# Performance work log

Measured on AMD Instinct MI355X. Metric: run time of the kernel, lower is better.

## Reference

```python
import jax, jax.numpy as jnp
import numpy as np

D_MODEL = 1024
NHEAD = 16
HEAD_DIM = D_MODEL // NHEAD  # 64
THETA = 10000.0


def apply_rope(t):
    # t: [B, H, S, D]. Interleaved-pair RoPE (lucidrains rotary-embedding-torch
    # rotate_queries_or_keys), positions = arange(S), theta = 10000.
    B, H, S, D = t.shape
    inv_freq = 1.0 / (THETA ** (jnp.arange(0, D, 2, dtype=jnp.float32) / D))  # [D/2]
    ang = jnp.arange(S, dtype=jnp.float32)[:, None] * inv_freq               # [S, D/2]
    cos = jnp.cos(ang).astype(t.dtype)
    sin = jnp.sin(ang).astype(t.dtype)
    tp = t.reshape(B, H, S, D // 2, 2)
    x1, x2 = tp[..., 0], tp[..., 1]
    rot = jnp.stack([x1 * cos - x2 * sin, x1 * sin + x2 * cos], axis=-1)
    return rot.reshape(B, H, S, D)


def setup_inputs() -> dict:
    key = jax.random.key(0)
    k0, k1, k2, k3, k4 = jax.random.split(key, 5)
    B, Sx, Sc = 2, 2048, 2048
    sc = 0.02  # weight init scale
    return {
        "x": jax.random.normal(k0, (B, Sx, D_MODEL), jnp.float32),
        "context": jax.random.normal(k1, (B, Sc, D_MODEL), jnp.float32),
        "Wq": jax.random.normal(k2, (D_MODEL, D_MODEL), jnp.float32) * sc,
        "Wv": jax.random.normal(k3, (D_MODEL, D_MODEL), jnp.float32) * sc,
        "Wo": jax.random.normal(k4, (D_MODEL, D_MODEL), jnp.float32) * sc,
        "bo": jnp.zeros((D_MODEL,), jnp.float32),
        "x_pos": jnp.arange(B * Sx, dtype=jnp.int64).reshape(B, Sx) % Sx,
        "context_pos": jnp.arange(B * Sc, dtype=jnp.int64).reshape(B, Sc) % Sc,
    }


def reference(x, context, Wq, Wv, Wo, bo, x_pos, context_pos):
    # x_pos/context_pos are unused when both streams use the internal
    # RotaryEmbedding (is_imu1=is_imu2=True), matching the original forward.
    B, Sx, _ = x.shape
    Sc = context.shape[1]
    q = (x @ Wq.T).reshape(B, Sx, NHEAD, HEAD_DIM).transpose(0, 2, 1, 3)
    # NOTE: original code uses projq (not projk) for keys — replicated here.
    k = (context @ Wq.T).reshape(B, Sc, NHEAD, HEAD_DIM).transpose(0, 2, 1, 3)
    v = (context @ Wv.T).reshape(B, Sc, NHEAD, HEAD_DIM).transpose(0, 2, 1, 3)
    q = apply_rope(q)
    k = apply_rope(k)
    scale = 1.0 / jnp.sqrt(jnp.asarray(HEAD_DIM, q.dtype))
    attn = jax.nn.softmax(jnp.einsum("bhqd,bhkd->bhqk", q, k) * scale, axis=-1)
    out = jnp.einsum("bhqk,bhkd->bhqd", attn, v)            # [B,H,Sx,hd]
    out = out.transpose(0, 2, 1, 3).reshape(B, Sx, D_MODEL)  # [B,Sx,d_model]
    return out @ Wo.T + bo
```

## Files before the change

### kernel.cpp

```cpp
#include <hip/hip_runtime.h>
#include <cmath>


typedef __bf16 bf16x8 __attribute__((ext_vector_type(8)));
typedef __bf16 bf16x4 __attribute__((ext_vector_type(4)));
typedef float f32x4 __attribute__((ext_vector_type(4)));
typedef float f32x16 __attribute__((ext_vector_type(16)));
typedef unsigned u32x4v __attribute__((ext_vector_type(4)));

#define MFMA(A, B, C) __builtin_amdgcn_mfma_f32_16x16x32_bf16(A, B, C, 0, 0, 0)
#define MFMA32(A, B, C) __builtin_amdgcn_mfma_f32_32x32x16_bf16(A, B, C, 0, 0, 0)
#define GLL16(g, l)                                                        \
  __builtin_amdgcn_global_load_lds(                                        \
      (const __attribute__((address_space(1))) unsigned int*)(g),          \
      (__attribute__((address_space(3))) unsigned int*)(l), 16, 0, 0)

__global__ __launch_bounds__(256) void cvt_all_kernel(
    const float* __restrict__ x, const float* __restrict__ ctx,
    const float* __restrict__ Wq, const float* __restrict__ Wv,
    const float* __restrict__ Wo, __bf16* __restrict__ xb, __bf16* __restrict__ cb,
    __bf16* __restrict__ Wqb, __bf16* __restrict__ Wvb, __bf16* __restrict__ Wob) {
  int base = blockIdx.x * 512 + threadIdx.x;
  const float* src;
  __bf16* dst;
  int off;
  if (base < 1048576) { src = x; dst = xb; off = 0; }
  else if (base < 2097152) { src = ctx; dst = cb; off = 1048576; }
  else if (base < 2359296) { src = Wq; dst = Wqb; off = 2097152; }
  else if (base < 2621440) { src = Wv; dst = Wvb; off = 2359296; }
  else { src = Wo; dst = Wob; off = 2621440; }
#pragma unroll
  for (int jj = 0; jj < 2; jj++) {
    int j = base - off + jj * 256;
    float4 f = ((const float4*)src)[j];
    bf16x4 o;
    o[0] = (__bf16)f.x; o[1] = (__bf16)f.y; o[2] = (__bf16)f.z; o[3] = (__bf16)f.w;
    ((bf16x4*)dst)[j] = o;
  }
}

__global__ __launch_bounds__(256) void gemm_proj(const __bf16* __restrict__ A0,
                                                 const __bf16* __restrict__ W0,
                                                 void* __restrict__ outQ,
                                                 void* __restrict__ outK,
                                                 void* __restrict__ outV) {
  const int tid = threadIdx.x;
  const int wave = tid >> 6, lane = tid & 63, quad = lane >> 4, l15 = lane & 15;
  const int mw = wave >> 1, nw = wave & 1;

  const int id = blockIdx.x;
  int m0, n0;
  const __bf16* A;
  const __bf16* W;
  bool vmode;
  if (id < 512) {
    const int xcd = id & 7, j = id >> 3;
    m0 = (xcd * 8 + (j & 7)) * 128;
    n0 = (j >> 3) * 128;
    A = A0;
    W = W0;
    vmode = false;
  } else {
    const int vid = id - 512;
    const int xcd = vid & 7, j = vid >> 3;
    m0 = (xcd * 4 + (j & 3)) * 128;
    n0 = (j >> 2) * 128;
    A = A0 + (size_t)4096 * 1024;
    W = W0 + (size_t)1024 * 1024;
    vmode = true;
  }

  __shared__ __attribute__((aligned(16))) __bf16 As[3][4096];
  __shared__ __attribute__((aligned(16))) __bf16 Ws[3][4096];

  int goff[2];
#pragma unroll
  for (int jj = 0; jj < 2; jj++) {
    const int s = jj * 256 + tid;
    const int row = s >> 2;
    const int kcg = (s & 3) ^ ((row >> 1) & 3);
    goff[jj] = row * 1024 + kcg * 8;
  }
  const __bf16* Ag = A + (size_t)m0 * 1024;
  const __bf16* Wg = W + (size_t)n0 * 1024;
  const int ldsoff0 = wave * 512;
  const int ldsoff1 = 2048 + wave * 512;

  const int sw = (l15 >> 1) & 3;
  int afoff[4], wfoff[4];
#pragma unroll
  for (int t = 0; t < 4; t++) {
    afoff[t] = (mw * 64 + t * 16 + l15) * 32 + (quad ^ sw) * 8;
    wfoff[t] = (nw * 64 + t * 16 + l15) * 32 + (quad ^ sw) * 8;
  }

  f32x4 acc[4][4] = {};

  auto stage = [&](int buf, int k0) {
    GLL16(Ag + goff[0] + k0, &As[buf][ldsoff0]);
    GLL16(Ag + goff[1] + k0, &As[buf][ldsoff1]);
    GLL16(Wg + goff[0] + k0, &Ws[buf][ldsoff0]);
    GLL16(Wg + goff[1] + k0, &Ws[buf][ldsoff1]);
  };
  auto compute = [&](int buf) {
    bf16x8 af[4], wf[4];
#pragma unroll
    for (int t = 0; t < 4; t++) af[t] = *(const bf16x8*)&As[buf][afoff[t]];
#pragma unroll
    for (int t = 0; t < 4; t++) wf[t] = *(const bf16x8*)&Ws[buf][wfoff[t]];
#pragma unroll
    for (int mt = 0; mt < 4; mt++)
#pragma unroll
      for (int nt = 0; nt < 4; nt++) acc[mt][nt] = MFMA(af[mt], wf[nt], acc[mt][nt]);
  };

  stage(0, 0);
  stage(1, 32);
  int buf = 0;
  for (int c = 0; c < 32; c++) {
    __syncthreads();
    if (c + 2 < 32) {
      int nb = buf + 2;
      if (nb >= 3) nb -= 3;
      stage(nb, (c + 2) * 32);
    }
    compute(buf);
    buf = (buf == 2) ? 0 : buf + 1;
  }

  if (!vmode) {
    const int isK = (m0 >= 4096);
    __bf16* O = (__bf16*)(isK ? outK : outQ);
    const float qsc = isK ? 1.0f : 0.18033688f;
    const int mb = m0 & 4095;
#pragma unroll
    for (int nt = 0; nt < 4; nt++) {
      const int n = n0 + nw * 64 + nt * 16 + l15;
      const int h = n >> 6, d = n & 63, p = d >> 1;
      const float invf_rev =
          __builtin_amdgcn_exp2f(-((float)p * 0.41524101f + 2.6514961f));
#pragma unroll
      for (int mt = 0; mt < 4; mt++) {
#pragma unroll
        for (int r = 0; r < 4; r++) {
          const int row = mb + mw * 64 + mt * 16 + quad * 4 + r;
          const int s = row & 2047, b = row >> 11;
          float v = acc[mt][nt][r];
          float pv = __shfl_xor(v, 1, 64);
          float fr = __builtin_amdgcn_fractf((float)s * invf_rev);
          float sn = __builtin_amdgcn_sinf(fr);
          float cs = __builtin_amdgcn_cosf(fr);
          float res = (lane & 1) ? (pv * sn + v * cs) : (v * cs - pv * sn);
          O[((size_t)(b * 16 + h) * 2048 + s) * 64 + d] = (__bf16)(res * qsc);
        }
      }
    }
  } else {
    __bf16* O = (__bf16*)outV;
#pragma unroll
    for (int nt = 0; nt < 4; nt++) {
      const int n = n0 + nw * 64 + nt * 16 + l15;
      const int h = n >> 6, d = n & 63;
#pragma unroll
      for (int mt = 0; mt < 4; mt++) {
        const int rowb = m0 + mw * 64 + mt * 16 + quad * 4;
        const int s = rowb & 2047, b = rowb >> 11;
        bf16x4 o;
#pragma unroll
        for (int r = 0; r < 4; r++) o[r] = (__bf16)acc[mt][nt][r];
        *(bf16x4*)(O + ((size_t)(b * 16 + h) * 64 + d) * 2048 + s) = o;
      }
    }
  }
}

__global__ __launch_bounds__(256) void gemm_out(const __bf16* __restrict__ A,
                                                const __bf16* __restrict__ W,
                                                float* __restrict__ O,
                                                const float* __restrict__ bias) {
  const int tid = threadIdx.x;
  const int wave = tid >> 6, lane = tid & 63, quad = lane >> 4, l15 = lane & 15;
  const int mw = wave >> 1, nw = wave & 1;
  const int id = blockIdx.x;
  const int xcd = id & 7, j = id >> 3;
  const int m0 = (xcd * 4 + (j & 3)) * 128;
  const int n0 = (j >> 2) * 64;

  __shared__ __attribute__((aligned(16))) __bf16 As[3][4096];
  __shared__ __attribute__((aligned(16))) __bf16 Ws[3][2048];

  int goff[2];
#pragma unroll
  for (int jj = 0; jj < 2; jj++) {
    const int s = jj * 256 + tid;
    const int row = s >> 2;
    const int kcg = (s & 3) ^ ((row >> 1) & 3);
    goff[jj] = row * 1024 + kcg * 8;
  }
  const int wrow = tid >> 2;
  const int wkcg = (tid & 3) ^ ((wrow >> 1) & 3);
  const int goffw = wrow * 1024 + wkcg * 8;

  const __bf16* Ag = A + (size_t)m0 * 1024;
  const __bf16* Wg = W + (size_t)n0 * 1024;
  const int ldsoff0 = wave * 512;
  const int ldsoff1 = 2048 + wave * 512;

  const int sw = (l15 >> 1) & 3;
  int afoff[4], wfoff[2];
#pragma unroll
  for (int t = 0; t < 4; t++)
    afoff[t] = (mw * 64 + t * 16 + l15) * 32 + (quad ^ sw) * 8;
#pragma unroll
  for (int t = 0; t < 2; t++)
    wfoff[t] = (nw * 32 + t * 16 + l15) * 32 + (quad ^ sw) * 8;

  f32x4 acc[4][2] = {};

  auto stage = [&](int buf, int k0) {
    GLL16(Ag + goff[0] + k0, &As[buf][ldsoff0]);
    GLL16(Ag + goff[1] + k0, &As[buf][ldsoff1]);
    GLL16(Wg + goffw + k0, &Ws[buf][ldsoff0]);
  };
  auto compute = [&](int buf) {
    bf16x8 af[4], wf[2];
#pragma unroll
    for (int t = 0; t < 4; t++) af[t] = *(const bf16x8*)&As[buf][afoff[t]];
#pragma unroll
    for (int t = 0; t < 2; t++) wf[t] = *(const bf16x8*)&Ws[buf][wfoff[t]];
#pragma unroll
    for (int mt = 0; mt < 4; mt++)
#pragma unroll
      for (int nt = 0; nt < 2; nt++) acc[mt][nt] = MFMA(af[mt], wf[nt], acc[mt][nt]);
  };

  stage(0, 0);
  stage(1, 32);
  int buf = 0;
  for (int c = 0; c < 32; c++) {
    __syncthreads();
    if (c + 2 < 32) {
      int nb = buf + 2;
      if (nb >= 3) nb -= 3;
      stage(nb, (c + 2) * 32);
    }
    compute(buf);
    buf = (buf == 2) ? 0 : buf + 1;
  }

#pragma unroll
  for (int nt = 0; nt < 2; nt++) {
    const int n = n0 + nw * 32 + nt * 16 + l15;
    const float bv = bias[n];
#pragma unroll
    for (int mt = 0; mt < 4; mt++) {
#pragma unroll
      for (int r = 0; r < 4; r++) {
        const int row = m0 + mw * 64 + mt * 16 + quad * 4 + r;
        O[(size_t)row * 1024 + n] = acc[mt][nt][r] + bv;
      }
    }
  }
}

__global__ __launch_bounds__(512, 4) void attn_kernel(const __bf16* __restrict__ Q,
                                                      const __bf16* __restrict__ K,
                                                      const __bf16* __restrict__ Vt,
                                                      __bf16* __restrict__ Aout) {
  const int tid = threadIdx.x;
  const int wave = tid >> 6, lane = tid & 63;
  const int l31 = lane & 31, hi = lane >> 5;
  const int qg = wave >> 1, kg = wave & 1;
  const int id = blockIdx.x;
  const int j = id >> 3;
  const int bh = ((id & 7) << 2) | (j & 3);
  const int q0 = (j >> 2) << 7;

  const __bf16* Qb = Q + (size_t)bh * (2048 * 64);
  const __bf16* Kb = K + (size_t)bh * (2048 * 64);
  const __bf16* Vb = Vt + (size_t)bh * (64 * 2048);

  __shared__ __attribute__((aligned(16))) __bf16 Kbuf[4][4096];
  __shared__ __attribute__((aligned(16))) __bf16 Vbuf[4][4096];

  bf16x8 qf[4];
  {
    const __bf16* qp = Qb + (size_t)(q0 + qg * 32 + l31) * 64 + hi * 8;
#pragma unroll
    for (int i = 0; i < 4; i++) qf[i] = *(const bf16x8*)(qp + i * 16);
  }

  const int s0 = wave * 64 + lane;
  const int r0 = s0 >> 3, c0 = (s0 & 7) ^ (r0 & 7);
  const __bf16* kgp = Kb + r0 * 64 + c0 * 8;
  const __bf16* vgp = Vb + r0 * 2048 + c0 * 8;
  const int klds = wave * 512;

  int koff[4];
  {
    const int rk = kg * 32 + l31;
#pragma unroll
    for (int i = 0; i < 4; i++) koff[i] = rk * 64 + (((2 * i + hi) ^ (rk & 7)) * 8);
  }
  int voff[2][2];
#pragma unroll
  for (int dt = 0; dt < 2; dt++) {
    const int rv = dt * 32 + l31;
#pragma unroll
    for (int ks = 0; ks < 2; ks++)
      voff[dt][ks] = rv * 64 + (((kg * 4 + ks * 2 + hi) ^ (rv & 7)) * 8);
  }

  f32x4 rs4 = {};
  f32x16 oacc[2] = {};

  auto stage = [&](int buf, int kt) {
    GLL16(kgp + kt * 64, &Kbuf[buf][klds]);
    GLL16(vgp + kt, &Vbuf[buf][klds]);
  };

  auto compute = [&](int buf) {
    f32x16 s = {};
#pragma unroll
    for (int i = 0; i < 4; i++) {
      bf16x8 kf = *(const bf16x8*)&Kbuf[buf][koff[i]];
      s = MFMA32(kf, qf[i], s);
    }
    float pe[16];
#pragma unroll
    for (int r = 0; r < 16; r++) pe[r] = __builtin_amdgcn_exp2f(s[r]);
#pragma unroll
    for (int r = 0; r < 16; r++) rs4[r & 3] += pe[r];
    bf16x8 pa[2];
#pragma unroll
    for (int sl = 0; sl < 2; sl++) {
      unsigned wa, wb, wc, wd;
      asm("v_cvt_pk_bf16_f32 %0, %1, %2" : "=v"(wa) : "v"(pe[8 * sl + 0]), "v"(pe[8 * sl + 1]));
      asm("v_cvt_pk_bf16_f32 %0, %1, %2" : "=v"(wb) : "v"(pe[8 * sl + 4]), "v"(pe[8 * sl + 5]));
      asm("v_cvt_pk_bf16_f32 %0, %1, %2" : "=v"(wc) : "v"(pe[8 * sl + 2]), "v"(pe[8 * sl + 3]));
      asm("v_cvt_pk_bf16_f32 %0, %1, %2" : "=v"(wd) : "v"(pe[8 * sl + 6]), "v"(pe[8 * sl + 7]));
      asm("v_permlane32_swap_b32 %0, %1" : "+v"(wa), "+v"(wb));
      asm("v_permlane32_swap_b32 %0, %1" : "+v"(wc), "+v"(wd));
      u32x4v t;
      t[0] = wa; t[1] = wc; t[2] = wb; t[3] = wd;
      pa[sl] = __builtin_bit_cast(bf16x8, t);
    }
#pragma unroll
    for (int dt = 0; dt < 2; dt++)
#pragma unroll
      for (int ks = 0; ks < 2; ks++) {
        bf16x8 vf = *(const bf16x8*)&Vbuf[buf][voff[dt][ks]];
        oacc[dt] = MFMA32(pa[ks], vf, oacc[dt]);
      }
  };

  stage(0, 0);
  stage(1, 64);
  for (int kt = 0; kt < 2048; kt += 128) {
    const int p = (kt >> 7) & 1;
    __syncthreads();
    if (kt + 128 < 2048) {
      stage(2 * (p ^ 1), kt + 128);
      stage(2 * (p ^ 1) + 1, kt + 192);
    }
    compute(2 * p);
    compute(2 * p + 1);
  }

  __syncthreads();
  float* Ored = (float*)&Kbuf[0][0];
  float* Lred = (float*)&Vbuf[0][0];

  float lw = (rs4[0] + rs4[1]) + (rs4[2] + rs4[3]);
  lw += __shfl_xor(lw, 32, 64);
  Lred[wave * 64 + lane] = lw;
  if (kg == 1) {
#pragma unroll
    for (int dt = 0; dt < 2; dt++)
#pragma unroll
      for (int r = 0; r < 16; r++)
        Ored[(qg * 32 + dt * 16 + r) * 64 + lane] = oacc[dt][r];
  }
  __syncthreads();
  if (kg == 0) {
    const int b = bh >> 4, h = bh & 15;
#pragma unroll
    for (int r = 0; r < 16; r++) {
      const int qrow = (r & 3) + 8 * (r >> 2) + 4 * hi;
      const float lt =
          Lred[(qg * 2) * 64 + qrow] + Lred[(qg * 2 + 1) * 64 + qrow];
      const float inv = 1.f / lt;
      const int qAbs = q0 + qg * 32 + qrow;
#pragma unroll
      for (int dt = 0; dt < 2; dt++) {
        const float o = oacc[dt][r] + Ored[(qg * 32 + dt * 16 + r) * 64 + lane];
        Aout[((size_t)(b * 2048 + qAbs)) * 1024 + h * 64 + dt * 32 + l31] =
            (__bf16)(o * inv);
      }
    }
  }
}

extern "C" void kernel_launch(void* const* d_in, const int* in_sizes, int n_in,
                              void* d_out, int out_size, void* d_ws, size_t ws_size,
                              hipStream_t stream) {
  const float* x   = (const float*)d_in[0];
  const float* ctx = (const float*)d_in[1];
  const float* Wq  = (const float*)d_in[2];
  const float* Wv  = (const float*)d_in[3];
  const float* Wo  = (const float*)d_in[4];
  const float* bo  = (const float*)d_in[5];

  char* ws = (char*)d_ws;
  const size_t MB = 1024 * 1024;
  __bf16* xb   = (__bf16*)(ws + 0 * MB);
  __bf16* cb   = (__bf16*)(ws + 8 * MB);
  __bf16* Wqb  = (__bf16*)(ws + 16 * MB);
  __bf16* Wvb  = (__bf16*)(ws + 18 * MB);
  __bf16* Wob  = (__bf16*)(ws + 20 * MB);
  __bf16* qh   = (__bf16*)(ws + 22 * MB);
  __bf16* kh   = (__bf16*)(ws + 30 * MB);
  __bf16* vt   = (__bf16*)(ws + 38 * MB);
  __bf16* attn = xb;

  cvt_all_kernel<<<5632, 256, 0, stream>>>(x, ctx, Wq, Wv, Wo, xb, cb, Wqb, Wvb, Wob);

  gemm_proj<<<768, 256, 0, stream>>>(xb, Wqb, (void*)qh, (void*)kh, (void*)vt);

  attn_kernel<<<512, 512, 0, stream>>>(qh, kh, vt, attn);

  gemm_out<<<512, 256, 0, stream>>>(attn, Wob, (float*)d_out, bo);
}
```

Measured before the change: 201.7 us.

## Deepen GEMM prefetch pipeline to four LDS stages with partial vmcnt waits

Both projection GEMMs (QKV and output) move from a three-buffer LDS ring to a four-buffer ring with three stages prefetched. The per-iteration __syncthreads is replaced by an explicit s_waitcnt vmcnt(N) plus barrier, so only the oldest stage must land while later global-to-LDS loads stay in flight. This targets exposed global memory latency that the implicit full vmcnt drain of __syncthreads caused. It costs more LDS per block, which may reduce occupancy, and relies on the hand-counted vmcnt values being correct.

```diff
diff --git a/kernel.cpp b/kernel.cpp
--- a/kernel.cpp
+++ b/kernel.cpp
@@ -14,6 +14,12 @@
   __builtin_amdgcn_global_load_lds(                                        \
       (const __attribute__((address_space(1))) unsigned int*)(g),          \
       (__attribute__((address_space(3))) unsigned int*)(l), 16, 0, 0)
+
+#define WAITB(N)                                          \
+  do {                                                    \
+    asm volatile("s_waitcnt vmcnt(" #N ")" ::: "memory"); \
+    __builtin_amdgcn_s_barrier();                         \
+  } while (0)
 
 __global__ __launch_bounds__(256) void cvt_all_kernel(
     const float* __restrict__ x, const float* __restrict__ ctx,
@@ -70,8 +76,8 @@
     vmode = true;
   }
 
-  __shared__ __attribute__((aligned(16))) __bf16 As[3][4096];
-  __shared__ __attribute__((aligned(16))) __bf16 Ws[3][4096];
+  __shared__ __attribute__((aligned(16))) __bf16 As[4][4096];
+  __shared__ __attribute__((aligned(16))) __bf16 Ws[4][4096];
 
   int goff[2];
 #pragma unroll
@@ -116,17 +122,16 @@
 
   stage(0, 0);
   stage(1, 32);
-  int buf = 0;
-  for (int c = 0; c < 32; c++) {
-    __syncthreads();
-    if (c + 2 < 32) {
-      int nb = buf + 2;
-      if (nb >= 3) nb -= 3;
-      stage(nb, (c + 2) * 32);
-    }
-    compute(buf);
-    buf = (buf == 2) ? 0 : buf + 1;
-  }
+  stage(2, 64);
+  for (int c = 0; c < 30; c++) {
+    WAITB(8);
+    if (c < 29) stage((c + 3) & 3, (c + 3) * 32);
+    compute(c & 3);
+  }
+  WAITB(4);
+  compute(2);
+  WAITB(0);
+  compute(3);
 
   if (!vmode) {
     const int isK = (m0 >= 4096);
@@ -186,8 +191,8 @@
   const int m0 = (xcd * 4 + (j & 3)) * 128;
   const int n0 = (j >> 2) * 64;
 
-  __shared__ __attribute__((aligned(16))) __bf16 As[3][4096];
-  __shared__ __attribute__((aligned(16))) __bf16 Ws[3][2048];
+  __shared__ __attribute__((aligned(16))) __bf16 As[4][4096];
+  __shared__ __attribute__((aligned(16))) __bf16 Ws[4][2048];
 
   int goff[2];
 #pragma unroll
@@ -236,17 +241,16 @@
 
   stage(0, 0);
   stage(1, 32);
-  int buf = 0;
-  for (int c = 0; c < 32; c++) {
-    __syncthreads();
-    if (c + 2 < 32) {
-      int nb = buf + 2;
-      if (nb >= 3) nb -= 3;
-      stage(nb, (c + 2) * 32);
-    }
-    compute(buf);
-    buf = (buf == 2) ? 0 : buf + 1;
-  }
+  stage(2, 64);
+  for (int c = 0; c < 30; c++) {
+    WAITB(6);
+    if (c < 29) stage((c + 3) & 3, (c + 3) * 32);
+    compute(c & 3);
+  }
+  WAITB(3);
+  compute(2);
+  WAITB(0);
+  compute(3);
 
 #pragma unroll
   for (int nt = 0; nt < 2; nt++) {
```

Measured after the change: 209.6 us. +3.9%, slower.
